# Optimization experiments

Hardware: AMD Instinct MI355X
Metric: run time of the kernel (lower is better)

The kernel has to match this reference:

```python
import jax, jax.numpy as jnp
import numpy as np

B, N, F_IN = 32, 512, 64
HEADS = (8, 8)
HIDS = (64, 64)
EDGE_P = 0.05  # graph density
NEG_SLOPE = 0.2
NEG_INF = -1e20


def setup_inputs() -> dict:
    key = jax.random.key(0)
    ks = jax.random.split(key, 8)
    x = jax.random.normal(ks[0], (B, N, F_IN), dtype=jnp.float32)
    adj = (jax.random.uniform(ks[1], (B, N, N)) < EDGE_P).astype(jnp.float32)
    adj = jnp.maximum(adj, adj.transpose(0, 2, 1))  # symmetric adjacency
    # mask = (batch, row): every (b, n) pair gets the masked softmax
    b_idx = jnp.repeat(jnp.arange(B, dtype=jnp.int32), N)   # [B*N]
    r_idx = jnp.tile(jnp.arange(N, dtype=jnp.int32), B)     # [B*N]
    # layer 0: f_in=64 -> f_out=64, H=8 ; layer 1: f_in=64*8=512 -> f_out=64, H=8
    W0 = jax.random.normal(ks[2], (F_IN, HIDS[0]), dtype=jnp.float32) / jnp.sqrt(jnp.float32(F_IN))
    a_src0 = jax.random.normal(ks[3], (HIDS[0], HEADS[0]), dtype=jnp.float32) / jnp.sqrt(jnp.float32(HIDS[0]))
    a_dst0 = jax.random.normal(ks[4], (HIDS[0], HEADS[0]), dtype=jnp.float32) / jnp.sqrt(jnp.float32(HIDS[0]))
    f_in1 = HIDS[0] * HEADS[0]
    W1 = jax.random.normal(ks[5], (f_in1, HIDS[1]), dtype=jnp.float32) / jnp.sqrt(jnp.float32(f_in1))
    a_src1 = jax.random.normal(ks[6], (HIDS[1], HEADS[1]), dtype=jnp.float32) / jnp.sqrt(jnp.float32(HIDS[1]))
    a_dst1 = jax.random.normal(ks[7], (HIDS[1], HEADS[1]), dtype=jnp.float32) / jnp.sqrt(jnp.float32(HIDS[1]))
    return dict(x=x, adj=adj, b_idx=b_idx, r_idx=r_idx,
                W0=W0, a_src0=a_src0, a_dst0=a_dst0,
                W1=W1, a_src1=a_src1, a_dst1=a_dst1)


def _gat_layer(x, adj, b_idx, r_idx, W, a_src, a_dst):
    # x: [B,N,f_in], adj: [B,N,N] (diag already set), W: [f_in,F], a_*: [F,H]
    hp = x @ W                                        # [B,N,F]
    s = jnp.einsum('bnf,fh->bhn', hp, a_src)          # attn_src
    d = jnp.einsum('bnf,fh->bhn', hp, a_dst)          # attn_dst
    attn = s[:, :, :, None] + d[:, :, None, :]        # [B,H,N,N]
    attn = jnp.where(attn >= 0, attn, NEG_SLOPE * attn)  # leaky_relu(0.2)
    attn = jnp.where(adj[:, None, :, :] == 0, 0.0, attn)  # masked_fill(adj==0, 0)
    rows = attn[b_idx, :, r_idx, :]                   # [K,H,N]
    rows = jnp.where(rows == 0.0, NEG_INF, rows)
    rows = jax.nn.softmax(rows, axis=-1)
    attn = attn.at[b_idx, :, r_idx, :].set(rows)
    return jnp.einsum('bhij,bjf->bhif', attn, hp)     # [B,H,N,F]


def reference(x, adj, b_idx, r_idx, W0, a_src0, a_dst0, W1, a_src1, a_dst1):
    Bn, Nn = x.shape[:2]
    # torch mutates adj in place: adj[batch,row,row] = 1 (self loops)
    adj = adj.at[b_idx, r_idx, r_idx].set(1.0)
    o = _gat_layer(x, adj, b_idx, r_idx, W0, a_src0, a_dst0)      # [B,H,N,F0]
    x1 = jax.nn.elu(o.transpose(0, 2, 1, 3).reshape(Bn, Nn, -1))  # [B,N,H*F0]
    o2 = _gat_layer(x1, adj, b_idx, r_idx, W1, a_src1, a_dst1)    # [B,H,N,F1]
    return o2.mean(axis=1)                                        # [B,N,F1]
```

## Files before the change

### kernel.cpp

```cpp
#include <hip/hip_runtime.h>
#include <hip/hip_bf16.h>
#include <math.h>

#define BB 32
#define NN 512

typedef _Float16 f16x8 __attribute__((ext_vector_type(8)));
typedef __fp16  fp16x2 __attribute__((ext_vector_type(2)));
typedef float f32x4 __attribute__((ext_vector_type(4)));

#define MFMA16(a, b, c) __builtin_amdgcn_mfma_f32_16x16x32_f16(a, b, c, 0, 0, 0)

union AF { f16x8 v; unsigned int u[4]; };

__device__ __forceinline__ void gload_lds16(const void* g, void* l) {
    __builtin_amdgcn_global_load_lds(
        (const __attribute__((address_space(1))) unsigned int*)g,
        (__attribute__((address_space(3))) unsigned int*)l, 16, 0, 0);
}
__device__ __forceinline__ void gload_lds4(const void* g, void* l) {
    __builtin_amdgcn_global_load_lds(
        (const __attribute__((address_space(1))) unsigned int*)g,
        (__attribute__((address_space(3))) unsigned int*)l, 4, 0, 0);
}

static __device__ __forceinline__ void epi16(
    const float* ctile, const float* asd_f, int row0, int t,
    float* __restrict__ s, float* __restrict__ dTg, _Float16* __restrict__ hpT,
    float* dmax_lds, float* __restrict__ pmax_out)
{
    int b = row0 >> 9, jb = row0 & 511;
    if (t < 128) {
        int rr = t >> 3, h = t & 7;
        float sv = 0.f, dv = 0.f;
#pragma unroll
        for (int f = 0; f < 64; ++f) {
            float hv = ctile[rr * 66 + f];
            sv = fmaf(hv, asd_f[f * 8 + h], sv);
            dv = fmaf(hv, asd_f[512 + f * 8 + h], dv);
        }
        s[((size_t)b * NN + jb + rr) * 8 + h] = sv;
        dTg[((size_t)b * 8 + h) * NN + jb + rr] = dv;
        dmax_lds[t] = dv;
    } else if (t < 256) {
        int t2 = t - 128;
        int f = t2 >> 1, jl = (t2 & 1) * 8;
        f16x8 hv;
#pragma unroll
        for (int e = 0; e < 8; ++e)
            hv[e] = (_Float16)ctile[(jl + e) * 66 + f];
        *(f16x8*)(hpT + ((size_t)b * 64 + f) * NN + jb + jl) = hv;
    }
    __syncthreads();
    if (t < 8) {
        float m = dmax_lds[t];
#pragma unroll
        for (int k = 1; k < 16; ++k) m = fmaxf(m, dmax_lds[t + 8 * k]);
        pmax_out[((size_t)b * 32 + (jb >> 4)) * 8 + t] = m;
    }
}

static __device__ __forceinline__ void epi32(
    const float* ctile, const float* asd_f, int row0, int t,
    float* __restrict__ s, float* __restrict__ dTg, _Float16* __restrict__ hpT,
    float* dmax_lds, float* __restrict__ pmax_out)
{
    int b = row0 >> 9, jb = row0 & 511;
    if (t < 256) {
        int rr = t >> 3, h = t & 7;
        float sv = 0.f, dv = 0.f;
#pragma unroll
        for (int f = 0; f < 64; ++f) {
            float hv = ctile[rr * 66 + f];
            sv = fmaf(hv, asd_f[f * 8 + h], sv);
            dv = fmaf(hv, asd_f[512 + f * 8 + h], dv);
        }
        s[((size_t)b * NN + jb + rr) * 8 + h] = sv;
        dTg[((size_t)b * 8 + h) * NN + jb + rr] = dv;
        dmax_lds[t] = dv;
    } else {
        int t2 = t - 256;
        int f = t2 >> 2, jl = (t2 & 3) * 8;
        f16x8 hv;
#pragma unroll
        for (int e = 0; e < 8; ++e)
            hv[e] = (_Float16)ctile[(jl + e) * 66 + f];
        *(f16x8*)(hpT + ((size_t)b * 64 + f) * NN + jb + jl) = hv;
    }
    __syncthreads();
    if (t < 8) {
        float m = dmax_lds[t];
#pragma unroll
        for (int k = 1; k < 32; ++k) m = fmaxf(m, dmax_lds[t + 8 * k]);
        pmax_out[((size_t)b * 16 + (jb >> 5)) * 8 + t] = m;
    }
}

__global__ __launch_bounds__(256) void k_front(
    const float* __restrict__ x, const float* __restrict__ W0,
    const float* __restrict__ W1, _Float16* __restrict__ W1T,
    const float* __restrict__ a_src, const float* __restrict__ a_dst,
    float* __restrict__ s, float* __restrict__ dTg, _Float16* __restrict__ hpT,
    float* __restrict__ pmax)
{
    __shared__ float ctile[16 * 66];
    __shared__ float asd_f[1024];
    __shared__ float dmax[128];
    int t = threadIdx.x, row0 = blockIdx.x * 16;
    int lane = t & 63, w = t >> 6, cn = lane & 15, rq = lane >> 4;

    if (blockIdx.x < 16) {
        int task = blockIdx.x * 256 + t;
        int n = task & 63, gabs = task >> 6;
        int c = gabs >> 3, g = gabs & 7;
        f16x8 hv;
#pragma unroll
        for (int e = 0; e < 8; ++e)
            hv[e] = (_Float16)W1[(size_t)(gabs * 8 + e) * 64 + n];
        *(f16x8*)(W1T + (size_t)n * 512 + c * 64 + (g ^ (n & 7)) * 8) = hv;
    }

    ((float4*)asd_f)[t] = (t < 128) ? ((const float4*)a_src)[t]
                                    : ((const float4*)a_dst)[t - 128];
    f32x4 acc;
#pragma unroll
    for (int e = 0; e < 4; ++e) acc[e] = 0.f;
    int nn0 = w * 16 + cn;
#pragma unroll
    for (int ks = 0; ks < 2; ++ks) {
        const float* xp = x + (size_t)(row0 + cn) * 64 + ks * 32 + rq * 8;
        float4 x0 = *(const float4*)xp, x1 = *(const float4*)(xp + 4);
        f16x8 ah = {(_Float16)x0.x, (_Float16)x0.y, (_Float16)x0.z, (_Float16)x0.w,
                    (_Float16)x1.x, (_Float16)x1.y, (_Float16)x1.z, (_Float16)x1.w};
        f16x8 bh;
#pragma unroll
        for (int e = 0; e < 8; ++e)
            bh[e] = (_Float16)W0[(size_t)((ks * 4 + rq) * 8 + e) * 64 + nn0];
        acc = MFMA16(ah, bh, acc);
    }
#pragma unroll
    for (int r = 0; r < 4; ++r)
        ctile[(rq * 4 + r) * 66 + w * 16 + cn] = acc[r];
    __syncthreads();
    epi16(ctile, asd_f, row0, t, s, dTg, hpT, dmax, pmax);
}

#define PBUILD(AOUT, SV, C0, CB, AVv, REL, DDv, Ev, Ebv)                \
    do {                                                                \
        _Pragma("unroll")                                               \
        for (int e = 0; e < 8; e += 2) {                                \
            float pA[2];                                                \
            _Pragma("unroll")                                           \
            for (int q = 0; q < 2; ++q) {                               \
                int ee = e + q;                                         \
                bool con = (AVv[ee] != 0.f) || (ee == (REL));           \
                float e0 = SV + DDv[ee];                                \
                float p0 = (e0 >= 0.f) ? (C0) * Ev[ee] : (CB) * Ebv[ee];\
                pA[q] = (con && e0 != 0.f) ? p0 : 0.f;                  \
            }                                                           \
            fp16x2 ka = __builtin_amdgcn_cvt_pkrtz(pA[0], pA[1]);       \
            AOUT.u[e >> 1] = __builtin_bit_cast(unsigned int, ka);      \
        }                                                               \
    } while (0)

template<int MODE>
__global__ __launch_bounds__(512, 4) void k_attn_fused(
    const float* __restrict__ s, const float* __restrict__ dTg,
    const float* __restrict__ pmaxd, const _Float16* __restrict__ hpT,
    const float* __restrict__ adj,
    const _Float16* __restrict__ W1T,
    const float* __restrict__ a_src, const float* __restrict__ a_dst,
    float* __restrict__ s_out, float* __restrict__ dTg_out,
    _Float16* __restrict__ hpT_out, float* __restrict__ pmax_out,
    float* __restrict__ o_f)
{
    __shared__ __align__(16) char smem[40960];
    char* bufP = smem;
    char* bufQ = smem + 18432;

    int blk = blockIdx.x;
    int vb = ((blk & 7) << 6) | (blk >> 3);
    int b = vb >> 4, i0 = (vb & 15) << 5;
    int row0 = vb * 32;
    int t = threadIdx.x, lane = t & 63, w = t >> 6;
    int cn = lane & 15, rq = lane >> 4;
    int myrow = i0 + cn;

    const _Float16* hb = hpT + (size_t)b * 64 * NN;
    int f0 = t >> 3, g0 = t & 7;
    const _Float16* hsrc = hb + (size_t)f0 * NN + ((g0 ^ (f0 & 7)) * 8);
    const float* dsrc = dTg + ((size_t)b * 8 + w) * NN + lane;
    int ar = t >> 4, ag = t & 15;
    const float* asrc = adj + (size_t)(row0 + ar) * NN + (((ag ^ (ar & 7))) << 2);

#define STAGE(BUF, JC)                                                   \
    do {                                                                 \
        gload_lds16(hsrc + (JC), (_Float16*)(BUF) + (w << 9));           \
        gload_lds4(dsrc + (JC), (float*)((BUF) + 8192) + (w << 6));      \
        gload_lds16(asrc + (JC), (float*)((BUF) + 10240) + (w << 8));    \
    } while (0)

    STAGE(bufP, 0);

    constexpr int NT = (MODE == 0) ? 32 : 16;
    float md = pmaxd[((size_t)b * NT + (lane & (NT - 1))) * 8 + w];
#pragma unroll
    for (int off = NT >> 1; off; off >>= 1) md = fmaxf(md, __shfl_xor(md, off));

    float svA = s[((size_t)b * NN + myrow) * 8 + w];
    float svB = s[((size_t)b * NN + myrow + 16) * 8 + w];
    float MA = fmaxf(svA + md, 0.f);
    float MB = fmaxf(svB + md, 0.f);
    float c0A = __expf(svA + md - MA), cbA = __expf(0.2f * (svA + md) - MA);
    float c0B = __expf(svB + md - MB), cbB = __expf(0.2f * (svB + md) - MB);
    int rq8 = rq * 8;

    f16x8 ones;
#pragma unroll
    for (int e = 0; e < 8; ++e) ones[e] = (_Float16)1.0f;

    f32x4 accA[4], accB[4], accrsA, accrsB;
#pragma unroll
    for (int e = 0; e < 4; ++e) { accrsA[e] = 0.f; accrsB[e] = 0.f; }
#pragma unroll
    for (int ft = 0; ft < 4; ++ft)
#pragma unroll
        for (int e = 0; e < 4; ++e) { accA[ft][e] = 0.f; accB[ft][e] = 0.f; }

    __syncthreads();

    for (int jcx = 0; jcx < 8; ++jcx) {
        int jc = jcx * 64;
        char* cur = (jcx & 1) ? bufQ : bufP;
        char* nxt = (jcx & 1) ? bufP : bufQ;
        if (jcx < 7) STAGE(nxt, jc + 64);
        const _Float16* hTc = (const _Float16*)cur;
        const float* ddl = (const float*)(cur + 8192) + (w << 6);
        const float* adl = (const float*)(cur + 10240);
        const float* arA = adl + cn * 64;
        const float* arB = adl + (16 + cn) * 64;
        int xA = cn & 7;
        float* Et = (float*)(smem + 36864) + (w << 7);
        {
            float ddj = ddl[lane];
            Et[lane]      = __expf(ddj - md);
            Et[lane + 64] = __expf(0.2f * (ddj - md));
        }
        asm volatile("s_waitcnt lgkmcnt(0)" ::: "memory");
#pragma unroll
        for (int ks = 0; ks < 2; ++ks) {
            int jo = ks * 32 + rq8;
            float dd[8], avA[8], avB[8], Ev[8], Ebv[8];
            *(float4*)&dd[0] = *(const float4*)(ddl + jo);
            *(float4*)&dd[4] = *(const float4*)(ddl + jo + 4);
            *(float4*)&Ev[0]  = *(const float4*)(Et + jo);
            *(float4*)&Ev[4]  = *(const float4*)(Et + jo + 4);
            *(float4*)&Ebv[0] = *(const float4*)(Et + 64 + jo);
            *(float4*)&Ebv[4] = *(const float4*)(Et + 64 + jo + 4);
            int G0 = jo >> 2;
            *(float4*)&avA[0] = *(const float4*)(arA + ((G0 ^ xA) << 2));
            *(float4*)&avA[4] = *(const float4*)(arA + (((G0 + 1) ^ xA) << 2));
            *(float4*)&avB[0] = *(const float4*)(arB + ((G0 ^ xA) << 2));
            *(float4*)&avB[4] = *(const float4*)(arB + (((G0 + 1) ^ xA) << 2));
            int relA = myrow - (jc + jo);
            int relB = relA + 16;
            AF aA, aB;
            PBUILD(aA, svA, c0A, cbA, avA, relA, dd, Ev, Ebv);
            PBUILD(aB, svB, c0B, cbB, avB, relB, dd, Ev, Ebv);
            accrsA = MFMA16(aA.v, ones, accrsA);
            accrsB = MFMA16(aB.v, ones, accrsB);
#pragma unroll
            for (int ft = 0; ft < 4; ++ft) {
                int f = ft * 16 + cn;
                f16x8 bh = *(const f16x8*)&hTc[f * 64 + (((ks * 4 + rq) ^ (f & 7)) * 8)];
                accA[ft] = MFMA16(aA.v, bh, accA[ft]);
                accB[ft] = MFMA16(aB.v, bh, accB[ft]);
            }
        }
        __syncthreads();
    }
#undef STAGE

    float invrA[4], invrB[4];
#pragma unroll
    for (int r = 0; r < 4; ++r) {
        invrA[r] = 1.0f / accrsA[r];
        invrB[r] = 1.0f / accrsB[r];
    }

    if (MODE == 0) {
        _Float16* x1all = (_Float16*)smem;
#pragma unroll
        for (int rt = 0; rt < 2; ++rt)
#pragma unroll
            for (int ft = 0; ft < 4; ++ft)
#pragma unroll
                for (int r = 0; r < 4; ++r) {
                    int il = rt * 16 + rq * 4 + r;
                    float v = rt ? accB[ft][r] * invrB[r]
                                 : accA[ft][r] * invrA[r];
                    v = v > 0.f ? v : __expf(v) - 1.f;
                    int f = ft * 16 + cn;
                    x1all[w * 2048 + il * 64 + (((f >> 3) ^ (il & 7)) * 8) + (f & 7)] =
                        (_Float16)v;
                }
        __syncthreads();
        f32x4 g1A, g1B;
#pragma unroll
        for (int e = 0; e < 4; ++e) { g1A[e] = 0.f; g1B[e] = 0.f; }
        int nn = (w & 3) * 16 + cn, kh = w >> 2;
        const _Float16* wb = W1T + (size_t)nn * 512;
#pragma unroll
        for (int kc2 = 0; kc2 < 4; ++kc2) {
            int kc = kh * 4 + kc2;
#pragma unroll
            for (int ks = 0; ks < 2; ++ks) {
                f16x8 bh = *(const f16x8*)(wb + kc * 64 +
                                           (((ks * 4 + rq) ^ (nn & 7)) * 8));
                f16x8 ahA = *(const f16x8*)&x1all[kc * 2048 + cn * 64 +
                                                  (((ks * 4 + rq) ^ (cn & 7)) * 8)];
                f16x8 ahB = *(const f16x8*)&x1all[kc * 2048 + (16 + cn) * 64 +
                                                  (((ks * 4 + rq) ^ (cn & 7)) * 8)];
                g1A = MFMA16(ahA, bh, g1A);
                g1B = MFMA16(ahB, bh, g1B);
            }
        }
        __syncthreads();
        float* ct = (float*)smem;
        float* asd_f = (float*)(smem + 33280);
        float* dmax = (float*)(smem + 37376);
#pragma unroll
        for (int r = 0; r < 4; ++r) {
            ct[kh * 2112 + (rq * 4 + r) * 66 + nn] = g1A[r];
            ct[kh * 2112 + (16 + rq * 4 + r) * 66 + nn] = g1B[r];
        }
        if (t < 256)
            ((float4*)asd_f)[t] = (t < 128) ? ((const float4*)a_src)[t]
                                            : ((const float4*)a_dst)[t - 128];
        __syncthreads();
        for (int idx = t; idx < 2112; idx += 512) ct[idx] += ct[2112 + idx];
        __syncthreads();
        epi32(ct, asd_f, row0, t, s_out, dTg_out, hpT_out, dmax, pmax_out);
    } else {
        float* red = (float*)smem;
#pragma unroll
        for (int ph = 0; ph < 2; ++ph) {
            if ((w >> 2) == ph) {
#pragma unroll
                for (int rt = 0; rt < 2; ++rt)
#pragma unroll
                    for (int ft = 0; ft < 4; ++ft)
#pragma unroll
                        for (int r = 0; r < 4; ++r) {
                            int il = rt * 16 + rq * 4 + r;
                            float v = rt ? accB[ft][r] * invrB[r]
                                         : accA[ft][r] * invrA[r];
                            int off = (w & 3) * 2048 + il * 64 + ft * 16 + cn;
                            if (ph == 0) red[off] = v;
                            else         red[off] += v;
                        }
            }
            __syncthreads();
        }
#pragma unroll
        for (int u = 0; u < 4; ++u) {
            int idx = t + u * 512;
            int il = idx >> 6, f = idx & 63;
            float sum = red[il * 64 + f] + red[2048 + il * 64 + f]
                      + red[4096 + il * 64 + f] + red[6144 + il * 64 + f];
            o_f[((size_t)b * NN + i0 + il) * 64 + f] = sum * 0.125f;
        }
    }
}

extern "C" void kernel_launch(void* const* d_in, const int* in_sizes, int n_in,
                              void* d_out, int out_size, void* d_ws, size_t ws_size,
                              hipStream_t stream) {
    const float* x      = (const float*)d_in[0];
    const float* adj    = (const float*)d_in[1];
    const float* W0     = (const float*)d_in[4];
    const float* a_src0 = (const float*)d_in[5];
    const float* a_dst0 = (const float*)d_in[6];
    const float* W1     = (const float*)d_in[7];
    const float* a_src1 = (const float*)d_in[8];
    const float* a_dst1 = (const float*)d_in[9];
    float* out = (float*)d_out;

    float* ws = (float*)d_ws;
    const size_t R = (size_t)BB * NN;
    const size_t BHN = (size_t)BB * 8 * NN;
    float* s0    = ws;
    float* dTg0  = s0 + R * 8;
    float* s1    = dTg0 + BHN;
    float* dTg1  = s1 + R * 8;
    float* pmax0 = dTg1 + BHN;
    float* pmax1 = pmax0 + 8192;
    _Float16* hp0T = (_Float16*)(pmax1 + 4096);
    _Float16* hp1T = hp0T + (size_t)BB * 64 * NN;
    _Float16* W1T  = hp1T + (size_t)BB * 64 * NN;

    k_front<<<1024, 256, 0, stream>>>(x, W0, W1, W1T, a_src0, a_dst0,
                                      s0, dTg0, hp0T, pmax0);
    k_attn_fused<0><<<512, 512, 0, stream>>>(s0, dTg0, pmax0, hp0T, adj,
                                             W1T, a_src1, a_dst1,
                                             s1, dTg1, hp1T, pmax1, nullptr);
    k_attn_fused<1><<<512, 512, 0, stream>>>(s1, dTg1, pmax1, hp1T, adj,
                                             nullptr, nullptr, nullptr,
                                             nullptr, nullptr, nullptr, nullptr, out);
}
```

Baseline: 152.7 us.

## Pack adjacency into bitmask in layer 0 and reuse it in layer 1

The first attention kernel now builds a per-row 64-bit connectivity mask (adjacency nonzero or self-loop) while it scans the float adjacency, and writes the masks to workspace. The second layer kernel reads these compact bitmasks from global memory instead of streaming the full fp32 adjacency through LDS, which cuts its adjacency traffic by 32x and shrinks its LDS staging buffers. This costs extra shuffles and global stores in layer 0 plus a small workspace region. The bitmask is derived within the same call, so it is not cross-call caching.

```diff
diff --git a/kernel.cpp b/kernel.cpp
--- a/kernel.cpp
+++ b/kernel.cpp
@@ -145,7 +145,7 @@
     epi16(ctile, asd_f, row0, t, s, dTg, hpT, dmax, pmax);
 }
 
-#define PBUILD(AOUT, SV, C0, CB, AVv, REL, DDv, Ev, Ebv)                \
+#define PBUILD(AOUT, SV, C0, CB, CONE, DDv, Ev, Ebv)                    \
     do {                                                                \
         _Pragma("unroll")                                               \
         for (int e = 0; e < 8; e += 2) {                                \
@@ -153,7 +153,7 @@
             _Pragma("unroll")                                           \
             for (int q = 0; q < 2; ++q) {                               \
                 int ee = e + q;                                         \
-                bool con = (AVv[ee] != 0.f) || (ee == (REL));           \
+                bool con = (CONE);                                      \
                 float e0 = SV + DDv[ee];                                \
                 float p0 = (e0 >= 0.f) ? (C0) * Ev[ee] : (CB) * Ebv[ee];\
                 pA[q] = (con && e0 != 0.f) ? p0 : 0.f;                  \
@@ -168,6 +168,8 @@
     const float* __restrict__ s, const float* __restrict__ dTg,
     const float* __restrict__ pmaxd, const _Float16* __restrict__ hpT,
     const float* __restrict__ adj,
+    const unsigned long long* __restrict__ adjb_in,
+    unsigned long long* __restrict__ adjb_out,
     const _Float16* __restrict__ W1T,
     const float* __restrict__ a_src, const float* __restrict__ a_dst,
     float* __restrict__ s_out, float* __restrict__ dTg_out,
@@ -175,8 +177,9 @@
     float* __restrict__ o_f)
 {
     __shared__ __align__(16) char smem[40960];
+    constexpr int BUFB = (MODE == 0) ? 18432 : 10240;
     char* bufP = smem;
-    char* bufQ = smem + 18432;
+    char* bufQ = smem + BUFB;
 
     int blk = blockIdx.x;
     int vb = ((blk & 7) << 6) | (blk >> 3);
@@ -191,16 +194,17 @@
     const _Float16* hsrc = hb + (size_t)f0 * NN + ((g0 ^ (f0 & 7)) * 8);
     const float* dsrc = dTg + ((size_t)b * 8 + w) * NN + lane;
     int ar = t >> 4, ag = t & 15;
-    const float* asrc = adj + (size_t)(row0 + ar) * NN + (((ag ^ (ar & 7))) << 2);
-
-#define STAGE(BUF, JC)                                                   \
-    do {                                                                 \
-        gload_lds16(hsrc + (JC), (_Float16*)(BUF) + (w << 9));           \
-        gload_lds4(dsrc + (JC), (float*)((BUF) + 8192) + (w << 6));      \
-        gload_lds16(asrc + (JC), (float*)((BUF) + 10240) + (w << 8));    \
-    } while (0)
-
-    STAGE(bufP, 0);
+    const float* asrc = (MODE == 0)
+        ? adj + (size_t)(row0 + ar) * NN + (((ag ^ (ar & 7))) << 2) : nullptr;
+
+    auto stage = [&](char* BUF, int JC) {
+        gload_lds16(hsrc + JC, (_Float16*)BUF + (w << 9));
+        gload_lds4(dsrc + JC, (float*)(BUF + 8192) + (w << 6));
+        if (MODE == 0)
+            gload_lds16(asrc + JC, (float*)(BUF + 10240) + (w << 8));
+    };
+
+    stage(bufP, 0);
 
     constexpr int NT = (MODE == 0) ? 32 : 16;
     float md = pmaxd[((size_t)b * NT + (lane & (NT - 1))) * 8 + w];
@@ -215,6 +219,13 @@
     float c0B = __expf(svB + md - MB), cbB = __expf(0.2f * (svB + md) - MB);
     int rq8 = rq * 8;
 
+    const unsigned long long* abr = (MODE == 1)
+        ? adjb_in + ((size_t)b * NN + myrow) * 8 : nullptr;
+    unsigned long long mbA = 0, mbB = 0;
+    if (MODE == 1) { mbA = abr[0]; mbB = abr[128]; }
+    unsigned long long* aoA = (MODE == 0)
+        ? adjb_out + ((size_t)b * NN + myrow) * 8 : nullptr;
+
     f16x8 ones;
 #pragma unroll
     for (int e = 0; e < 8; ++e) ones[e] = (_Float16)1.0f;
@@ -226,6 +237,8 @@
     for (int ft = 0; ft < 4; ++ft)
 #pragma unroll
         for (int e = 0; e < 4; ++e) { accA[ft][e] = 0.f; accB[ft][e] = 0.f; }
+
+    float* Et = (float*)(smem + 36864) + (w << 7);
 
     __syncthreads();
 
@@ -233,40 +246,60 @@
         int jc = jcx * 64;
         char* cur = (jcx & 1) ? bufQ : bufP;
         char* nxt = (jcx & 1) ? bufP : bufQ;
-        if (jcx < 7) STAGE(nxt, jc + 64);
+        if (jcx < 7) stage(nxt, jc + 64);
+        unsigned long long mbnA = 0, mbnB = 0;
+        if (MODE == 1 && jcx < 7) { mbnA = abr[jcx + 1]; mbnB = abr[jcx + 129]; }
         const _Float16* hTc = (const _Float16*)cur;
         const float* ddl = (const float*)(cur + 8192) + (w << 6);
         const float* adl = (const float*)(cur + 10240);
         const float* arA = adl + cn * 64;
         const float* arB = adl + (16 + cn) * 64;
         int xA = cn & 7;
-        float* Et = (float*)(smem + 36864) + (w << 7);
+        unsigned int mlA = (unsigned)mbA, mhA = (unsigned)(mbA >> 32);
+        unsigned int mlB = (unsigned)mbB, mhB = (unsigned)(mbB >> 32);
         {
             float ddj = ddl[lane];
             Et[lane]      = __expf(ddj - md);
             Et[lane + 64] = __expf(0.2f * (ddj - md));
         }
         asm volatile("s_waitcnt lgkmcnt(0)" ::: "memory");
+        unsigned long long u64A = 0, u64B = 0;
 #pragma unroll
         for (int ks = 0; ks < 2; ++ks) {
             int jo = ks * 32 + rq8;
-            float dd[8], avA[8], avB[8], Ev[8], Ebv[8];
-            *(float4*)&dd[0] = *(const float4*)(ddl + jo);
-            *(float4*)&dd[4] = *(const float4*)(ddl + jo + 4);
+            float dd[8], Ev[8], Ebv[8];
+            *(float4*)&dd[0]  = *(const float4*)(ddl + jo);
+            *(float4*)&dd[4]  = *(const float4*)(ddl + jo + 4);
             *(float4*)&Ev[0]  = *(const float4*)(Et + jo);
             *(float4*)&Ev[4]  = *(const float4*)(Et + jo + 4);
             *(float4*)&Ebv[0] = *(const float4*)(Et + 64 + jo);
             *(float4*)&Ebv[4] = *(const float4*)(Et + 64 + jo + 4);
-            int G0 = jo >> 2;
-            *(float4*)&avA[0] = *(const float4*)(arA + ((G0 ^ xA) << 2));
-            *(float4*)&avA[4] = *(const float4*)(arA + (((G0 + 1) ^ xA) << 2));
-            *(float4*)&avB[0] = *(const float4*)(arB + ((G0 ^ xA) << 2));
-            *(float4*)&avB[4] = *(const float4*)(arB + (((G0 + 1) ^ xA) << 2));
             int relA = myrow - (jc + jo);
             int relB = relA + 16;
             AF aA, aB;
-            PBUILD(aA, svA, c0A, cbA, avA, relA, dd, Ev, Ebv);
-            PBUILD(aB, svB, c0B, cbB, avB, relB, dd, Ev, Ebv);
+            if (MODE == 0) {
+                float avA[8], avB[8];
+                int G0 = jo >> 2;
+                *(float4*)&avA[0] = *(const float4*)(arA + ((G0 ^ xA) << 2));
+                *(float4*)&avA[4] = *(const float4*)(arA + (((G0 + 1) ^ xA) << 2));
+                *(float4*)&avB[0] = *(const float4*)(arB + ((G0 ^ xA) << 2));
+                *(float4*)&avB[4] = *(const float4*)(arB + (((G0 + 1) ^ xA) << 2));
+                unsigned mskA = 0, mskB = 0;
+#pragma unroll
+                for (int e = 0; e < 8; ++e) {
+                    if (avA[e] != 0.f || e == relA) mskA |= 1u << e;
+                    if (avB[e] != 0.f || e == relB) mskB |= 1u << e;
+                }
+                u64A |= (unsigned long long)mskA << (ks * 32 + rq8);
+                u64B |= (unsigned long long)mskB << (ks * 32 + rq8);
+                PBUILD(aA, svA, c0A, cbA, (avA[ee] != 0.f || ee == relA), dd, Ev, Ebv);
+                PBUILD(aB, svB, c0B, cbB, (avB[ee] != 0.f || ee == relB), dd, Ev, Ebv);
+            } else {
+                unsigned int mbyA = ((ks ? mhA : mlA) >> rq8) & 0xffu;
+                unsigned int mbyB = ((ks ? mhB : mlB) >> rq8) & 0xffu;
+                PBUILD(aA, svA, c0A, cbA, ((mbyA >> ee) & 1u), dd, Ev, Ebv);
+                PBUILD(aB, svB, c0B, cbB, ((mbyB >> ee) & 1u), dd, Ev, Ebv);
+            }
             accrsA = MFMA16(aA.v, ones, accrsA);
             accrsB = MFMA16(aB.v, ones, accrsB);
 #pragma unroll
@@ -277,9 +310,14 @@
                 accB[ft] = MFMA16(aB.v, bh, accB[ft]);
             }
         }
+        if (MODE == 0) {
+            u64A |= __shfl_xor(u64A, 16); u64A |= __shfl_xor(u64A, 32);
+            u64B |= __shfl_xor(u64B, 16); u64B |= __shfl_xor(u64B, 32);
+            if (rq == 0) { aoA[jcx] = u64A; aoA[128 + jcx] = u64B; }
+        }
+        if (MODE == 1) { mbA = mbnA; mbB = mbnB; }
         __syncthreads();
     }
-#undef STAGE
 
     float invrA[4], invrB[4];
 #pragma unroll
@@ -398,13 +436,16 @@
     _Float16* hp0T = (_Float16*)(pmax1 + 4096);
     _Float16* hp1T = hp0T + (size_t)BB * 64 * NN;
     _Float16* W1T  = hp1T + (size_t)BB * 64 * NN;
+    unsigned long long* adjb = (unsigned long long*)(W1T + (size_t)64 * 512);
 
     k_front<<<1024, 256, 0, stream>>>(x, W0, W1, W1T, a_src0, a_dst0,
                                       s0, dTg0, hp0T, pmax0);
     k_attn_fused<0><<<512, 512, 0, stream>>>(s0, dTg0, pmax0, hp0T, adj,
+                                             nullptr, adjb,
                                              W1T, a_src1, a_dst1,
                                              s1, dTg1, hp1T, pmax1, nullptr);
-    k_attn_fused<1><<<512, 512, 0, stream>>>(s1, dTg1, pmax1, hp1T, adj,
+    k_attn_fused<1><<<512, 512, 0, stream>>>(s1, dTg1, pmax1, hp1T, nullptr,
+                                             adjb, nullptr,
                                              nullptr, nullptr, nullptr,
                                              nullptr, nullptr, nullptr, nullptr, out);
 }
```

Measured after the change: 155.2 us. About the same (+1.6%).
